# Kernel optimization log

Hardware: AMD Instinct MI355X
Metric: run time of the kernel (lower is better)

## Reference

```python
import jax, jax.numpy as jnp
import numpy as np

EPS = 1e-10


def setup_inputs() -> dict:
    key = jax.random.key(0)
    k1, k2, k3 = jax.random.split(key, 3)
    N, D, K = 16384, 512, 8192
    x = jax.random.normal(k1, (N, D), dtype=jnp.float32)
    # trunc_normal(std=0.2) init approximated by clipped normal
    codebook = jnp.clip(0.2 * jax.random.normal(k2, (K, D), dtype=jnp.float32), -0.4, 0.4)
    gumbel_u = jax.random.uniform(k3, (N, K), dtype=jnp.float32)
    temperature = jnp.float32(0.7)
    return {"x": x, "codebook": codebook, "gumbel_u": gumbel_u, "temperature": temperature}


def reference(x, codebook, gumbel_u, temperature):
    # squared euclidean distance via sum-of-squares + matmul: [N, K]
    x2 = jnp.sum(x * x, axis=1, keepdims=True)              # [N, 1]
    c2 = jnp.sum(codebook * codebook, axis=1)               # [K]
    dist = x2 + c2[None, :] - 2.0 * (x @ codebook.T)        # [N, K]
    ids = jnp.argmax(-dist, axis=1)                         # [N]
    # gumbel-softmax sample over -dist logits
    g = -jnp.log(-jnp.log(gumbel_u + EPS) + EPS)            # gumbel noise [N, K]
    weights = jax.nn.softmax((-dist + g) / temperature, axis=1)
    emb = weights @ codebook                                # [N, D]
    return emb, ids
```

## Files before the change

### kernel.cpp

```cpp
#include <hip/hip_runtime.h>

#define NROWS 16384
#define DIM   512
#define BM    32
#define KTILE 32
#define NT    256
#define KC    8192
#define QCAP  32768
#define MARGIN 0.05f
#define DEFER_THR 8.0f
#define LN2   0.69314718055994531f

typedef _Float16 half8  __attribute__((ext_vector_type(8)));
typedef float    f32x4  __attribute__((ext_vector_type(4)));
typedef unsigned int u32;

#define MFMA(a,b,c) __builtin_amdgcn_mfma_f32_16x16x32_f16(a,b,c,0,0,0)

__device__ __forceinline__ float flog2(float x){ return __builtin_amdgcn_logf(x); }
__device__ __forceinline__ float fexp2(float x){ return __builtin_amdgcn_exp2f(x); }
__device__ __forceinline__ f32x4 ntload4(const float* p){
  return __builtin_nontemporal_load((const f32x4*)p);
}
__device__ __forceinline__ void gload16(const void* g, void* l){
  __builtin_amdgcn_global_load_lds(
      (const __attribute__((address_space(1))) u32*)g,
      (__attribute__((address_space(3))) u32*)l, 16, 0, 0);
}

__device__ __forceinline__ void top2_merge(float& v1, int& i1, float& v2, int& i2,
                                           float bv1, int bi1, float bv2, int bi2) {
  bool takeB = (bv1 > v1) || (bv1 == v1 && bi1 < i1);
  float nv1 = takeB ? bv1 : v1; int ni1 = takeB ? bi1 : i1;
  float cv  = takeB ? v1  : bv1; int ci = takeB ? i1  : bi1;
  float ov2 = takeB ? bv2 : v2;  int oi = takeB ? bi2 : i2;
  bool cb = (cv > ov2) || (cv == ov2 && ci < oi);
  v2 = cb ? cv : ov2; i2 = cb ? ci : oi;
  v1 = nv1; i1 = ni1;
}

__global__ void prep_x(const float* __restrict__ x, _Float16* __restrict__ xh) {
  size_t i = (size_t)(blockIdx.x * blockDim.x + threadIdx.x) * 4;
  f32x4 v = *(const f32x4*)(x + i);
  _Float16 h4[4];
  h4[0] = (_Float16)(2.0f * v[0]); h4[1] = (_Float16)(2.0f * v[1]);
  h4[2] = (_Float16)(2.0f * v[2]); h4[3] = (_Float16)(2.0f * v[3]);
  *(uint2*)(xh + i) = *(uint2*)h4;
}

__global__ void prep_cht(const float* __restrict__ c, _Float16* __restrict__ cht) {
  const int gid = blockIdx.x * 256 + threadIdx.x;
  const int code = gid >> 6, u = gid & 63;
  f32x4 v0 = *(const f32x4*)(c + (size_t)code * DIM + u * 8);
  f32x4 v1 = *(const f32x4*)(c + (size_t)code * DIM + u * 8 + 4);
  half8 h;
#pragma unroll
  for (int q = 0; q < 4; ++q) { h[q] = (_Float16)v0[q]; h[4+q] = (_Float16)v1[q]; }
  const int t = code >> 5, cc = code & 31;
  *(half8*)((char*)cht + (size_t)t * 32768 + cc * 1024 + ((u ^ (cc & 7)) << 4)) = h;
}

__global__ void prep_ctt(const float* __restrict__ c, _Float16* __restrict__ ctt) {
  __shared__ _Float16 lt[64][72];
  const int kb = (blockIdx.x >> 3) * 64;
  const int db = (blockIdx.x & 7) * 64;
  {
    const int r = threadIdx.x >> 2, c4 = threadIdx.x & 3;
#pragma unroll
    for (int j = 0; j < 4; ++j) {
      f32x4 v = *(const f32x4*)(c + (size_t)(kb + r) * DIM + db + c4 * 16 + j * 4);
#pragma unroll
      for (int q = 0; q < 4; ++q) lt[r][c4 * 16 + j * 4 + q] = (_Float16)v[q];
    }
  }
  __syncthreads();
  {
    const int d = threadIdx.x >> 2, ks = threadIdx.x & 3;
    half8 o0, o1;
#pragma unroll
    for (int j = 0; j < 8; ++j) { o0[j] = lt[ks*16 + j][d]; o1[j] = lt[ks*16 + 8 + j][d]; }
    const int dg = db + d;
    const int t = (kb >> 5) + (ks >> 1);
    const int u0 = (ks & 1) * 2;
    char* base = (char*)ctt + (size_t)t * 32768 + (size_t)dg * 64;
    *(half8*)(base + ((u0       ^ (dg & 3)) << 4)) = o0;
    *(half8*)(base + (((u0 + 1) ^ (dg & 3)) << 4)) = o1;
  }
}

__global__ void prep_c2(const float* __restrict__ c, float* __restrict__ c2) {
  const int w = threadIdx.x >> 6, l = threadIdx.x & 63;
  const int code = blockIdx.x * 4 + w;
  double s = 0.0;
  for (int i = l; i < DIM; i += 64) { double v = c[(size_t)code * DIM + i]; s += v * v; }
#pragma unroll
  for (int o = 32; o; o >>= 1) s += __shfl_down(s, o, 64);
  if (l == 0) c2[code] = (float)s;
}

__global__ __launch_bounds__(256, 2) void vq_fused(
    const float* __restrict__ U, const _Float16* __restrict__ Xh,
    const _Float16* __restrict__ CHT, const _Float16* __restrict__ CTT,
    const float* __restrict__ C2, const float* __restrict__ Tp,
    float* __restrict__ emb, float* __restrict__ ids,
    int* __restrict__ fixcnt, int* __restrict__ fixq) {
  __shared__ __align__(16) char smem[71680];
  const int tid = threadIdx.x;
  const int w = tid >> 6, l = tid & 63, l15 = l & 15, l4 = l >> 4;
  const int cs = w & 1, rs = w >> 1;
  const int row0 = blockIdx.x * BM;
  const float c1 = 1.4426950408889634f / Tp[0];
  const char* CHTc = (const char*)CHT;
  const char* CTTc = (const char*)CTT;

  half8 xr[16];
  {
    const _Float16* xb = Xh + (size_t)(row0 + rs*16 + l15) * DIM + l4 * 8;
#pragma unroll
    for (int kc = 0; kc < 16; ++kc) xr[kc] = *(const half8*)(xb + kc * 32);
  }

  const int sxq = l15 & 7;
  const int sxp = (l15 ^ (l15 >> 2)) & 3;
  const int qkb = (cs*16 + l15) * 1024;
  const int prow = rs*16 + l15;

  const float* ub  = U  + (size_t)(row0 + prow) * KC + cs*16 + l4*4;
  const float* c2p = C2 + cs*16 + l4*4;

  f32x4 upre  = ntload4(ub);
  f32x4 c2pre = *(const f32x4*)(c2p);

  {
    const char* g = CHTc + (size_t)(w*64 + l) * 16;
    char* lb = smem + w * 1024;
#pragma unroll
    for (int r = 0; r < 8; ++r) gload16(g + r * 4096, lb + r * 4096);
  }

  f32x4 O[8][2];
#pragma unroll
  for (int a = 0; a < 8; ++a)
#pragma unroll
    for (int b = 0; b < 2; ++b) { O[a][b][0]=0.f; O[a][b][1]=0.f; O[a][b][2]=0.f; O[a][b][3]=0.f; }
  half8 ctf[8];
  float mO[2] = {-3e38f, -3e38f};
  float l_run = 0.f;
  float v1 = -3e38f, v2 = -3e38f; int i1 = 0, i2 = 0;
  float* mtab = (float*)(smem + 69632);

  __syncthreads();

#pragma unroll 1
  for (int t = 0; t < NT; ++t) {
    const char* chc = smem + ((t & 1) << 15);

    if (t < NT - 1) {
      const char* g = CHTc + ((size_t)(t + 1)) * 32768 + (size_t)(w*64 + l) * 16;
      char* lb = smem + (((t + 1) & 1) << 15) + w * 1024;
#pragma unroll
      for (int r = 0; r < 8; ++r) gload16(g + r * 4096, lb + r * 4096);
    }

    f32x4 a0 = {0.f, 0.f, 0.f, 0.f};
#pragma unroll
    for (int kc = 0; kc < 16; ++kc) {
      half8 A0 = *(const half8*)(chc + qkb + (((kc*4 + l4) ^ sxq) << 4));
      a0 = MFMA(A0, xr[kc], a0);
    }

    f32x4 zz; float mw = -3e38f;
    {
      const int cbase = t*32 + cs*16 + l4*4;
#pragma unroll
      for (int r = 0; r < 4; ++r) {
        float s = a0[r] - c2pre[r];
        if (s > v1) { v2 = v1; i2 = i1; v1 = s; i1 = cbase + r; }
        else if (s > v2) { v2 = s; i2 = cbase + r; }
        float li = flog2(upre[r] + 1e-10f);
        float y  = fmaf(li, -LN2, 1e-10f);
        float g  = flog2(y) * (-LN2);
        float z  = (s + g) * c1;
        zz[r] = z;
        mw = fmaxf(mw, z);
      }
    }
    mw = fmaxf(mw, __shfl_xor(mw, 16, 64));
    mw = fmaxf(mw, __shfl_xor(mw, 32, 64));
    if (l < 16) mtab[w*16 + l] = mw;

    asm volatile("s_waitcnt lgkmcnt(0)" ::: "memory");
    __builtin_amdgcn_s_barrier();
    __builtin_amdgcn_sched_barrier(0);

    float alphaO[2];
#pragma unroll
    for (int rt = 0; rt < 2; ++rt) {
      float mt = fmaxf(mtab[(2*rt)*16 + l15], mtab[(2*rt + 1)*16 + l15]);
      float mo = mO[rt];
      float mn = (mt > mo + DEFER_THR) ? mt : mo;
      alphaO[rt] = fexp2(mo - mn);
      mO[rt] = mn;
    }
    const float m_own = rs ? mO[1] : mO[0];
    const float a_own = rs ? alphaO[1] : alphaO[0];

    if (t < NT - 1) {
      upre  = ntload4(ub + (size_t)(t + 1) * 32);
      c2pre = *(const f32x4*)(c2p + (t + 1) * 32);
    }

    {
      char* pcur = smem + 65536 + ((t & 1) << 11);
      float p0 = fexp2(zz[0] - m_own);
      float p1 = fexp2(zz[1] - m_own);
      float p2 = fexp2(zz[2] - m_own);
      float p3 = fexp2(zz[3] - m_own);
      l_run = l_run * a_own + ((p0 + p1) + (p2 + p3));
      const int u = cs*2 + (l4 >> 1);
      union { _Float16 h[4]; uint2 q; } pk;
      pk.h[0] = (_Float16)p0; pk.h[1] = (_Float16)p1;
      pk.h[2] = (_Float16)p2; pk.h[3] = (_Float16)p3;
      *(uint2*)(pcur + prow*64 + ((u ^ sxp) << 4) + ((l4 & 1) << 3)) = pk.q;
    }

    if (t > 0) {
      const char* pprev = smem + 65536 + (((t - 1) & 1) << 11);
      half8 pf0 = *(const half8*)(pprev + l15*64        + ((l4 ^ sxp) << 4));
      half8 pf1 = *(const half8*)(pprev + (16 + l15)*64 + ((l4 ^ sxp) << 4));
#pragma unroll
      for (int dt = 0; dt < 8; ++dt) {
        O[dt][0] = MFMA(ctf[dt], pf0, O[dt][0]);
        O[dt][1] = MFMA(ctf[dt], pf1, O[dt][1]);
      }
    }

#pragma unroll
    for (int dt = 0; dt < 8; ++dt)
      ctf[dt] = *(const half8*)(CTTc + (size_t)t * 32768
                                + (size_t)(w*128 + dt*16 + l15) * 64
                                + ((l4 ^ (l15 & 3)) << 4));

#pragma unroll
    for (int rt = 0; rt < 2; ++rt) {
      if (__any(alphaO[rt] != 1.0f)) {
        const float a_ = alphaO[rt];
#pragma unroll
        for (int dt = 0; dt < 8; ++dt) {
          O[dt][rt][0] *= a_; O[dt][rt][1] *= a_;
          O[dt][rt][2] *= a_; O[dt][rt][3] *= a_;
        }
      }
    }

    __builtin_amdgcn_sched_barrier(0);
    asm volatile("s_waitcnt vmcnt(10) lgkmcnt(0)" ::: "memory");
    __builtin_amdgcn_s_barrier();
    __builtin_amdgcn_sched_barrier(0);
  }

  {
    const char* pprev = smem + 65536 + (((NT - 1) & 1) << 11);
    half8 pf0 = *(const half8*)(pprev + l15*64        + ((l4 ^ sxp) << 4));
    half8 pf1 = *(const half8*)(pprev + (16 + l15)*64 + ((l4 ^ sxp) << 4));
#pragma unroll
    for (int dt = 0; dt < 8; ++dt) {
      O[dt][0] = MFMA(ctf[dt], pf0, O[dt][0]);
      O[dt][1] = MFMA(ctf[dt], pf1, O[dt][1]);
    }
  }

  float lt2 = l_run;
  lt2 += __shfl_xor(lt2, 16, 64);
  lt2 += __shfl_xor(lt2, 32, 64);
  {
    float bv1 = __shfl_xor(v1, 16, 64); int bi1 = __shfl_xor(i1, 16, 64);
    float bv2 = __shfl_xor(v2, 16, 64); int bi2 = __shfl_xor(i2, 16, 64);
    top2_merge(v1, i1, v2, i2, bv1, bi1, bv2, bi2);
    bv1 = __shfl_xor(v1, 32, 64); bi1 = __shfl_xor(i1, 32, 64);
    bv2 = __shfl_xor(v2, 32, 64); bi2 = __shfl_xor(i2, 32, 64);
    top2_merge(v1, i1, v2, i2, bv1, bi1, bv2, bi2);
  }
  float* ltab = (float*)(smem + 69888);
  f32x4* atab = (f32x4*)(smem + 70144);
  if (l < 16) {
    ltab[w*16 + l] = lt2;
    f32x4 pk;
    pk[0] = v1; pk[1] = __int_as_float(i1); pk[2] = v2; pk[3] = __int_as_float(i2);
    atab[w*16 + l] = pk;
  }
  __syncthreads();

  const float invr0 = 1.0f / (ltab[l15] + ltab[16 + l15]);
  const float invr1 = 1.0f / (ltab[32 + l15] + ltab[48 + l15]);

  if (w == 0 && l < 32) {
    const int rt = l >> 4, r15 = l & 15;
    f32x4 A = atab[(2*rt)*16 + r15];
    f32x4 B = atab[(2*rt + 1)*16 + r15];
    float V1 = A[0], V2 = A[2];
    int I1 = __float_as_int(A[1]), I2 = __float_as_int(A[3]);
    top2_merge(V1, I1, V2, I2, B[0], __float_as_int(B[1]), B[2], __float_as_int(B[3]));
    ids[row0 + l] = (float)I1;
    if (V1 - V2 <= MARGIN) {
      int qi = atomicAdd(fixcnt, 1);
      if (qi < QCAP) { fixq[qi*3] = row0 + l; fixq[qi*3 + 1] = I1; fixq[qi*3 + 2] = I2; }
    }
  }

  float* stagef = (float*)smem;
#pragma unroll
  for (int h = 0; h < 2; ++h) {
    __syncthreads();
    const float iv = h ? invr1 : invr0;
#pragma unroll
    for (int dt = 0; dt < 8; ++dt) {
      f32x4 v = O[dt][h];
      v[0] *= iv; v[1] *= iv; v[2] *= iv; v[3] *= iv;
      *(f32x4*)(stagef + l15*520 + w*128 + dt*16 + l4*4) = v;
    }
    __syncthreads();
#pragma unroll
    for (int q = 0; q < 8; ++q) {
      const int c = q*256 + tid;
      const int r_ = c >> 7, col = c & 127;
      f32x4 v = *(const f32x4*)(stagef + r_*520 + col*4);
      __builtin_nontemporal_store(v,
          (f32x4*)(emb + (size_t)(row0 + h*16 + r_)*DIM + col*4));
    }
  }
}

__global__ void vq_fixup(const float* __restrict__ X, const float* __restrict__ C,
                         const int* __restrict__ fixcnt, const int* __restrict__ fixq,
                         float* __restrict__ ids) {
  const int nw = (gridDim.x * blockDim.x) >> 6;
  const int gw = (blockIdx.x * blockDim.x + threadIdx.x) >> 6;
  const int l = threadIdx.x & 63;
  int cnt = *fixcnt; if (cnt > QCAP) cnt = QCAP;
  for (int q = gw; q < cnt; q += nw) {
    const int row = fixq[q*3], a = fixq[q*3 + 1], b = fixq[q*3 + 2];
    double da = 0, ca = 0, db = 0, cb = 0;
    for (int i = l; i < DIM; i += 64) {
      double xv = X[(size_t)row * DIM + i];
      double av = C[(size_t)a * DIM + i];
      double bv = C[(size_t)b * DIM + i];
      da += xv * av; ca += av * av;
      db += xv * bv; cb += bv * bv;
    }
#pragma unroll
    for (int o = 32; o; o >>= 1) {
      da += __shfl_down(da, o, 64); ca += __shfl_down(ca, o, 64);
      db += __shfl_down(db, o, 64); cb += __shfl_down(cb, o, 64);
    }
    if (l == 0) {
      double sa = 2.0 * da - ca, sb = 2.0 * db - cb;
      int win = (sb > sa || (sb == sa && b < a)) ? b : a;
      ids[row] = (float)win;
    }
  }
}

extern "C" void kernel_launch(void* const* d_in, const int* in_sizes, int n_in,
                              void* d_out, int out_size, void* d_ws, size_t ws_size,
                              hipStream_t stream) {
  (void)in_sizes; (void)n_in; (void)out_size; (void)ws_size;
  const float* x  = (const float*)d_in[0];
  const float* cb = (const float*)d_in[1];
  const float* u  = (const float*)d_in[2];
  const float* tp = (const float*)d_in[3];
  float* emb = (float*)d_out;
  float* ids = emb + (size_t)NROWS * DIM;

  char* ws = (char*)d_ws;
  int* fixcnt = (int*)ws;
  int* fixq = (int*)(ws + 256);
  size_t off = (256 + (size_t)QCAP * 12 + 511) & ~(size_t)511;
  _Float16* xh  = (_Float16*)(ws + off); off += (size_t)NROWS * DIM * 2;
  _Float16* cht = (_Float16*)(ws + off); off += (size_t)KC * DIM * 2;
  _Float16* ctt = (_Float16*)(ws + off); off += (size_t)DIM * KC * 2;
  float* c2 = (float*)(ws + off);

  hipMemsetAsync(fixcnt, 0, 4, stream);
  prep_x  <<<(NROWS * DIM) / 1024, 256, 0, stream>>>(x, xh);
  prep_cht<<<(KC * 64) / 256, 256, 0, stream>>>(cb, cht);
  prep_ctt<<<(KC / 64) * (DIM / 64), 256, 0, stream>>>(cb, ctt);
  prep_c2 <<<KC / 4, 256, 0, stream>>>(cb, c2);
  vq_fused<<<NROWS / BM, 256, 0, stream>>>(u, xh, cht, ctt, c2, tp, emb, ids, fixcnt, fixq);
  vq_fixup<<<32, 256, 0, stream>>>(x, cb, fixcnt, fixq, ids);
}
```

Measured before the change: 620.7 us.

## Double row tile to 64 with 512-thread blocks sharing codebook tiles

Doubles the rows per block from 32 to 64 and launches 8 waves per block, so each staged codebook tile in LDS and each CTT fragment is reused across twice as many rows. Each wave now owns 64 output dims across 4 row-tiles, holding an O[4][4] accumulator, and tracks its own softmax max separately. The distance MFMA chain is split into two independent accumulators, and the epilogue writes through per-wave LDS staging with no block-wide sync. In exchange it raises register pressure and shared memory per block, which may reduce occupancy.

```diff
diff --git a/kernel.cpp b/kernel.cpp
--- a/kernel.cpp
+++ b/kernel.cpp
@@ -2,7 +2,7 @@
 
 #define NROWS 16384
 #define DIM   512
-#define BM    32
+#define BM    64
 #define KTILE 32
 #define NT    256
 #define KC    8192
@@ -98,13 +98,13 @@
   if (l == 0) c2[code] = (float)s;
 }
 
-__global__ __launch_bounds__(256, 2) void vq_fused(
+__global__ __launch_bounds__(512, 2) void vq_fused(
     const float* __restrict__ U, const _Float16* __restrict__ Xh,
     const _Float16* __restrict__ CHT, const _Float16* __restrict__ CTT,
     const float* __restrict__ C2, const float* __restrict__ Tp,
     float* __restrict__ emb, float* __restrict__ ids,
     int* __restrict__ fixcnt, int* __restrict__ fixq) {
-  __shared__ __align__(16) char smem[71680];
+  __shared__ __align__(16) char smem[76800];
   const int tid = threadIdx.x;
   const int w = tid >> 6, l = tid & 63, l15 = l & 15, l4 = l >> 4;
   const int cs = w & 1, rs = w >> 1;
@@ -121,9 +121,12 @@
   }
 
   const int sxq = l15 & 7;
+  const int qkb = (cs*16 + l15) * 1024;
+  const int eE = ((l4      ) ^ sxq) << 4;
+  const int eO = ((4 | l4  ) ^ sxq) << 4;
   const int sxp = (l15 ^ (l15 >> 2)) & 3;
-  const int qkb = (cs*16 + l15) * 1024;
   const int prow = rs*16 + l15;
+  const int cxo = (l4 ^ (l15 & 3)) << 4;
 
   const float* ub  = U  + (size_t)(row0 + prow) * KC + cs*16 + l4*4;
   const float* c2p = C2 + cs*16 + l4*4;
@@ -132,22 +135,22 @@
   f32x4 c2pre = *(const f32x4*)(c2p);
 
   {
-    const char* g = CHTc + (size_t)(w*64 + l) * 16;
-    char* lb = smem + w * 1024;
-#pragma unroll
-    for (int r = 0; r < 8; ++r) gload16(g + r * 4096, lb + r * 4096);
-  }
-
-  f32x4 O[8][2];
-#pragma unroll
-  for (int a = 0; a < 8; ++a)
-#pragma unroll
-    for (int b = 0; b < 2; ++b) { O[a][b][0]=0.f; O[a][b][1]=0.f; O[a][b][2]=0.f; O[a][b][3]=0.f; }
-  half8 ctf[8];
-  float mO[2] = {-3e38f, -3e38f};
-  float l_run = 0.f;
+    const char* g = CHTc + (size_t)tid * 16;
+    char* lb = smem + (size_t)tid * 16;
+#pragma unroll
+    for (int r = 0; r < 4; ++r) gload16(g + r * 8192, lb + r * 8192);
+  }
+
+  f32x4 O[4][4];
+#pragma unroll
+  for (int a = 0; a < 4; ++a)
+#pragma unroll
+    for (int b = 0; b < 4; ++b) { O[a][b][0]=0.f; O[a][b][1]=0.f; O[a][b][2]=0.f; O[a][b][3]=0.f; }
+  half8 ctf[4];
+  float mO[4] = {-3e38f, -3e38f, -3e38f, -3e38f};
+  float m_own = -3e38f, l_run = 0.f;
   float v1 = -3e38f, v2 = -3e38f; int i1 = 0, i2 = 0;
-  float* mtab = (float*)(smem + 69632);
+  float* mtab = (float*)(smem + 73728);
 
   __syncthreads();
 
@@ -156,18 +159,28 @@
     const char* chc = smem + ((t & 1) << 15);
 
     if (t < NT - 1) {
-      const char* g = CHTc + ((size_t)(t + 1)) * 32768 + (size_t)(w*64 + l) * 16;
-      char* lb = smem + (((t + 1) & 1) << 15) + w * 1024;
-#pragma unroll
-      for (int r = 0; r < 8; ++r) gload16(g + r * 4096, lb + r * 4096);
-    }
-
-    f32x4 a0 = {0.f, 0.f, 0.f, 0.f};
-#pragma unroll
-    for (int kc = 0; kc < 16; ++kc) {
-      half8 A0 = *(const half8*)(chc + qkb + (((kc*4 + l4) ^ sxq) << 4));
-      a0 = MFMA(A0, xr[kc], a0);
-    }
+      const char* g = CHTc + ((size_t)(t + 1)) * 32768 + (size_t)tid * 16;
+      char* lb = smem + (((t + 1) & 1) << 15) + (size_t)tid * 16;
+#pragma unroll
+      for (int r = 0; r < 4; ++r) gload16(g + r * 8192, lb + r * 8192);
+    }
+    __builtin_amdgcn_sched_barrier(0);
+
+    f32x4 ae = {0.f,0.f,0.f,0.f}, ao = {0.f,0.f,0.f,0.f};
+    {
+      const char* pE = chc + qkb + eE;
+      const char* pO = chc + qkb + eO;
+#pragma unroll
+      for (int j = 0; j < 8; ++j) {
+        half8 AE = *(const half8*)(pE + j * 128);
+        half8 AO = *(const half8*)(pO + j * 128);
+        ae = MFMA(AE, xr[2*j],     ae);
+        ao = MFMA(AO, xr[2*j + 1], ao);
+      }
+    }
+    f32x4 a0;
+    a0[0] = ae[0] + ao[0]; a0[1] = ae[1] + ao[1];
+    a0[2] = ae[2] + ao[2]; a0[3] = ae[3] + ao[3];
 
     f32x4 zz; float mw = -3e38f;
     {
@@ -193,17 +206,21 @@
     __builtin_amdgcn_s_barrier();
     __builtin_amdgcn_sched_barrier(0);
 
-    float alphaO[2];
-#pragma unroll
-    for (int rt = 0; rt < 2; ++rt) {
+    float alphaO[4];
+#pragma unroll
+    for (int rt = 0; rt < 4; ++rt) {
       float mt = fmaxf(mtab[(2*rt)*16 + l15], mtab[(2*rt + 1)*16 + l15]);
       float mo = mO[rt];
       float mn = (mt > mo + DEFER_THR) ? mt : mo;
       alphaO[rt] = fexp2(mo - mn);
       mO[rt] = mn;
     }
-    const float m_own = rs ? mO[1] : mO[0];
-    const float a_own = rs ? alphaO[1] : alphaO[0];
+    {
+      float mt = fmaxf(mtab[(2*rs)*16 + l15], mtab[(2*rs + 1)*16 + l15]);
+      float mn = (mt > m_own + DEFER_THR) ? mt : m_own;
+      l_run *= fexp2(m_own - mn);
+      m_own = mn;
+    }
 
     if (t < NT - 1) {
       upre  = ntload4(ub + (size_t)(t + 1) * 32);
@@ -211,12 +228,12 @@
     }
 
     {
-      char* pcur = smem + 65536 + ((t & 1) << 11);
+      char* pcur = smem + 65536 + ((t & 1) << 12);
       float p0 = fexp2(zz[0] - m_own);
       float p1 = fexp2(zz[1] - m_own);
       float p2 = fexp2(zz[2] - m_own);
       float p3 = fexp2(zz[3] - m_own);
-      l_run = l_run * a_own + ((p0 + p1) + (p2 + p3));
+      l_run += (p0 + p1) + (p2 + p3);
       const int u = cs*2 + (l4 >> 1);
       union { _Float16 h[4]; uint2 q; } pk;
       pk.h[0] = (_Float16)p0; pk.h[1] = (_Float16)p1;
@@ -225,28 +242,31 @@
     }
 
     if (t > 0) {
-      const char* pprev = smem + 65536 + (((t - 1) & 1) << 11);
-      half8 pf0 = *(const half8*)(pprev + l15*64        + ((l4 ^ sxp) << 4));
-      half8 pf1 = *(const half8*)(pprev + (16 + l15)*64 + ((l4 ^ sxp) << 4));
-#pragma unroll
-      for (int dt = 0; dt < 8; ++dt) {
-        O[dt][0] = MFMA(ctf[dt], pf0, O[dt][0]);
-        O[dt][1] = MFMA(ctf[dt], pf1, O[dt][1]);
-      }
-    }
-
-#pragma unroll
-    for (int dt = 0; dt < 8; ++dt)
-      ctf[dt] = *(const half8*)(CTTc + (size_t)t * 32768
-                                + (size_t)(w*128 + dt*16 + l15) * 64
-                                + ((l4 ^ (l15 & 3)) << 4));
-
-#pragma unroll
-    for (int rt = 0; rt < 2; ++rt) {
+      const char* pprev = smem + 65536 + (((t - 1) & 1) << 12);
+      half8 pf[4];
+#pragma unroll
+      for (int rt = 0; rt < 4; ++rt)
+        pf[rt] = *(const half8*)(pprev + (rt*16 + l15)*64 + ((l4 ^ sxp) << 4));
+#pragma unroll
+      for (int dt = 0; dt < 4; ++dt)
+#pragma unroll
+        for (int rt = 0; rt < 4; ++rt)
+          O[dt][rt] = MFMA(ctf[dt], pf[rt], O[dt][rt]);
+    }
+
+    {
+      const char* cb_ = CTTc + (size_t)t * 32768 + (size_t)(w*64 + l15) * 64 + cxo;
+#pragma unroll
+      for (int dt = 0; dt < 4; ++dt)
+        ctf[dt] = *(const half8*)(cb_ + dt * 1024);
+    }
+
+#pragma unroll
+    for (int rt = 0; rt < 4; ++rt) {
       if (__any(alphaO[rt] != 1.0f)) {
         const float a_ = alphaO[rt];
 #pragma unroll
-        for (int dt = 0; dt < 8; ++dt) {
+        for (int dt = 0; dt < 4; ++dt) {
           O[dt][rt][0] *= a_; O[dt][rt][1] *= a_;
           O[dt][rt][2] *= a_; O[dt][rt][3] *= a_;
         }
@@ -254,20 +274,22 @@
     }
 
     __builtin_amdgcn_sched_barrier(0);
-    asm volatile("s_waitcnt vmcnt(10) lgkmcnt(0)" ::: "memory");
+    asm volatile("s_waitcnt vmcnt(6) lgkmcnt(0)" ::: "memory");
     __builtin_amdgcn_s_barrier();
     __builtin_amdgcn_sched_barrier(0);
   }
 
   {
-    const char* pprev = smem + 65536 + (((NT - 1) & 1) << 11);
-    half8 pf0 = *(const half8*)(pprev + l15*64        + ((l4 ^ sxp) << 4));
-    half8 pf1 = *(const half8*)(pprev + (16 + l15)*64 + ((l4 ^ sxp) << 4));
-#pragma unroll
-    for (int dt = 0; dt < 8; ++dt) {
-      O[dt][0] = MFMA(ctf[dt], pf0, O[dt][0]);
-      O[dt][1] = MFMA(ctf[dt], pf1, O[dt][1]);
-    }
+    const char* pprev = smem + 65536 + (((NT - 1) & 1) << 12);
+    half8 pf[4];
+#pragma unroll
+    for (int rt = 0; rt < 4; ++rt)
+      pf[rt] = *(const half8*)(pprev + (rt*16 + l15)*64 + ((l4 ^ sxp) << 4));
+#pragma unroll
+    for (int dt = 0; dt < 4; ++dt)
+#pragma unroll
+      for (int rt = 0; rt < 4; ++rt)
+        O[dt][rt] = MFMA(ctf[dt], pf[rt], O[dt][rt]);
   }
 
   float lt2 = l_run;
@@ -281,8 +303,8 @@
     bv2 = __shfl_xor(v2, 32, 64); bi2 = __shfl_xor(i2, 32, 64);
     top2_merge(v1, i1, v2, i2, bv1, bi1, bv2, bi2);
   }
-  float* ltab = (float*)(smem + 69888);
-  f32x4* atab = (f32x4*)(smem + 70144);
+  float* ltab = (float*)(smem + 74240);
+  f32x4* atab = (f32x4*)(smem + 74752);
   if (l < 16) {
     ltab[w*16 + l] = lt2;
     f32x4 pk;
@@ -291,13 +313,14 @@
   }
   __syncthreads();
 
-  const float invr0 = 1.0f / (ltab[l15] + ltab[16 + l15]);
-  const float invr1 = 1.0f / (ltab[32 + l15] + ltab[48 + l15]);
-
-  if (w == 0 && l < 32) {
-    const int rt = l >> 4, r15 = l & 15;
-    f32x4 A = atab[(2*rt)*16 + r15];
-    f32x4 B = atab[(2*rt + 1)*16 + r15];
+  float inv4[4];
+#pragma unroll
+  for (int rt = 0; rt < 4; ++rt)
+    inv4[rt] = 1.0f / (ltab[(2*rt)*16 + l15] + ltab[(2*rt + 1)*16 + l15]);
+
+  if (w == 0) {
+    f32x4 A = atab[(2*(l >> 4))*16 + (l & 15)];
+    f32x4 B = atab[(2*(l >> 4) + 1)*16 + (l & 15)];
     float V1 = A[0], V2 = A[2];
     int I1 = __float_as_int(A[1]), I2 = __float_as_int(A[3]);
     top2_merge(V1, I1, V2, I2, B[0], __float_as_int(B[1]), B[2], __float_as_int(B[3]));
@@ -308,25 +331,28 @@
     }
   }
 
-  float* stagef = (float*)smem;
+  char* wbase = smem + w * 9216;
 #pragma unroll
   for (int h = 0; h < 2; ++h) {
-    __syncthreads();
-    const float iv = h ? invr1 : invr0;
-#pragma unroll
-    for (int dt = 0; dt < 8; ++dt) {
-      f32x4 v = O[dt][h];
-      v[0] *= iv; v[1] *= iv; v[2] *= iv; v[3] *= iv;
-      *(f32x4*)(stagef + l15*520 + w*128 + dt*16 + l4*4) = v;
-    }
-    __syncthreads();
-#pragma unroll
-    for (int q = 0; q < 8; ++q) {
-      const int c = q*256 + tid;
-      const int r_ = c >> 7, col = c & 127;
-      f32x4 v = *(const f32x4*)(stagef + r_*520 + col*4);
-      __builtin_nontemporal_store(v,
-          (f32x4*)(emb + (size_t)(row0 + h*16 + r_)*DIM + col*4));
+#pragma unroll
+    for (int rtl = 0; rtl < 2; ++rtl) {
+      const int rt = 2*h + rtl;
+      const int lrow = rtl*16 + l15;
+#pragma unroll
+      for (int dt = 0; dt < 4; ++dt)
+#pragma unroll
+        for (int r = 0; r < 4; ++r) {
+          const int dloc = dt*16 + l4*4 + r;
+          *(float*)(wbase + (lrow*72 + dloc)*4) = O[dt][rt][r] * inv4[rt];
+        }
+    }
+    __builtin_amdgcn_s_waitcnt(0);
+#pragma unroll
+    for (int ir = 0; ir < 8; ++ir) {
+      const int lrow = ir*4 + l4;
+      f32x4 vv = *(const f32x4*)(wbase + (lrow*72 + l15*4)*4);
+      __builtin_nontemporal_store(vv,
+          (f32x4*)(emb + (size_t)(row0 + h*32 + lrow)*DIM + w*64 + l15*4));
     }
   }
 }
@@ -386,6 +412,6 @@
   prep_cht<<<(KC * 64) / 256, 256, 0, stream>>>(cb, cht);
   prep_ctt<<<(KC / 64) * (DIM / 64), 256, 0, stream>>>(cb, ctt);
   prep_c2 <<<KC / 4, 256, 0, stream>>>(cb, c2);
-  vq_fused<<<NROWS / BM, 256, 0, stream>>>(u, xh, cht, ctt, c2, tp, emb, ids, fixcnt, fixq);
+  vq_fused<<<NROWS / BM, 512, 0, stream>>>(u, xh, cht, ctt, c2, tp, emb, ids, fixcnt, fixq);
   vq_fixup<<<32, 256, 0, stream>>>(x, cb, fixcnt, fixq, ids);
 }
```

Result: no change. 631.0 us (+1.7%).

## Load codebook fragments directly into registers instead of staging through LDS

Applied to the files above, without the earlier changes.

The fp16 codebook tile is re-laid out in the prep kernel so that each lane can load its MFMA A-fragments straight from global memory into registers. These registers are prefetched one tile ahead, replacing the double-buffered global_load_lds path and cutting shared memory from about 70KB to about 39KB. The distance MFMA chain is split into two independent accumulators to shorten the dependency chain. The cost is 16 extra half8 registers per lane and global latency exposed through register prefetch, with possible register pressure under the 2-waves launch bound. Two waves per column slice now fetch the same data from global or L2 rather than sharing one LDS copy.

```diff
diff --git a/kernel.cpp b/kernel.cpp
--- a/kernel.cpp
+++ b/kernel.cpp
@@ -3,7 +3,6 @@
 #define NROWS 16384
 #define DIM   512
 #define BM    32
-#define KTILE 32
 #define NT    256
 #define KC    8192
 #define QCAP  32768
@@ -13,7 +12,6 @@
 
 typedef _Float16 half8  __attribute__((ext_vector_type(8)));
 typedef float    f32x4  __attribute__((ext_vector_type(4)));
-typedef unsigned int u32;
 
 #define MFMA(a,b,c) __builtin_amdgcn_mfma_f32_16x16x32_f16(a,b,c,0,0,0)
 
@@ -21,11 +19,6 @@
 __device__ __forceinline__ float fexp2(float x){ return __builtin_amdgcn_exp2f(x); }
 __device__ __forceinline__ f32x4 ntload4(const float* p){
   return __builtin_nontemporal_load((const f32x4*)p);
-}
-__device__ __forceinline__ void gload16(const void* g, void* l){
-  __builtin_amdgcn_global_load_lds(
-      (const __attribute__((address_space(1))) u32*)g,
-      (__attribute__((address_space(3))) u32*)l, 16, 0, 0);
 }
 
 __device__ __forceinline__ void top2_merge(float& v1, int& i1, float& v2, int& i2,
@@ -48,7 +41,7 @@
   *(uint2*)(xh + i) = *(uint2*)h4;
 }
 
-__global__ void prep_cht(const float* __restrict__ c, _Float16* __restrict__ cht) {
+__global__ void prep_cht2(const float* __restrict__ c, _Float16* __restrict__ cht) {
   const int gid = blockIdx.x * 256 + threadIdx.x;
   const int code = gid >> 6, u = gid & 63;
   f32x4 v0 = *(const f32x4*)(c + (size_t)code * DIM + u * 8);
@@ -56,8 +49,8 @@
   half8 h;
 #pragma unroll
   for (int q = 0; q < 4; ++q) { h[q] = (_Float16)v0[q]; h[4+q] = (_Float16)v1[q]; }
-  const int t = code >> 5, cc = code & 31;
-  *(half8*)((char*)cht + (size_t)t * 32768 + cc * 1024 + ((u ^ (cc & 7)) << 4)) = h;
+  const int t = code >> 5, cc = code & 31, kc = u >> 2, ul = u & 3;
+  *(half8*)((char*)cht + (size_t)t * 32768 + kc * 2048 + cc * 64 + ul * 16) = h;
 }
 
 __global__ void prep_ctt(const float* __restrict__ c, _Float16* __restrict__ ctt) {
@@ -100,17 +93,17 @@
 
 __global__ __launch_bounds__(256, 2) void vq_fused(
     const float* __restrict__ U, const _Float16* __restrict__ Xh,
-    const _Float16* __restrict__ CHT, const _Float16* __restrict__ CTT,
+    const _Float16* __restrict__ CHT2, const _Float16* __restrict__ CTT,
     const float* __restrict__ C2, const float* __restrict__ Tp,
     float* __restrict__ emb, float* __restrict__ ids,
     int* __restrict__ fixcnt, int* __restrict__ fixq) {
-  __shared__ __align__(16) char smem[71680];
+  __shared__ __align__(16) char smem[39936];
   const int tid = threadIdx.x;
   const int w = tid >> 6, l = tid & 63, l15 = l & 15, l4 = l >> 4;
   const int cs = w & 1, rs = w >> 1;
   const int row0 = blockIdx.x * BM;
   const float c1 = 1.4426950408889634f / Tp[0];
-  const char* CHTc = (const char*)CHT;
+  const char* CH2c = (const char*)CHT2;
   const char* CTTc = (const char*)CTT;
 
   half8 xr[16];
@@ -120,10 +113,9 @@
     for (int kc = 0; kc < 16; ++kc) xr[kc] = *(const half8*)(xb + kc * 32);
   }
 
-  const int sxq = l15 & 7;
   const int sxp = (l15 ^ (l15 >> 2)) & 3;
-  const int qkb = (cs*16 + l15) * 1024;
   const int prow = rs*16 + l15;
+  const int afo = (cs*16 + l15) * 64 + l4*16;
 
   const float* ub  = U  + (size_t)(row0 + prow) * KC + cs*16 + l4*4;
   const float* c2p = C2 + cs*16 + l4*4;
@@ -131,12 +123,10 @@
   f32x4 upre  = ntload4(ub);
   f32x4 c2pre = *(const f32x4*)(c2p);
 
-  {
-    const char* g = CHTc + (size_t)(w*64 + l) * 16;
-    char* lb = smem + w * 1024;
-#pragma unroll
-    for (int r = 0; r < 8; ++r) gload16(g + r * 4096, lb + r * 4096);
-  }
+  half8 af[16];
+#pragma unroll
+  for (int kc = 0; kc < 16; ++kc)
+    af[kc] = *(const half8*)(CH2c + kc * 2048 + afo);
 
   f32x4 O[8][2];
 #pragma unroll
@@ -147,26 +137,28 @@
   float mO[2] = {-3e38f, -3e38f};
   float l_run = 0.f;
   float v1 = -3e38f, v2 = -3e38f; int i1 = 0, i2 = 0;
-  float* mtab = (float*)(smem + 69632);
+  float* mtab = (float*)(smem + 37888);
 
   __syncthreads();
 
 #pragma unroll 1
   for (int t = 0; t < NT; ++t) {
-    const char* chc = smem + ((t & 1) << 15);
-
-    if (t < NT - 1) {
-      const char* g = CHTc + ((size_t)(t + 1)) * 32768 + (size_t)(w*64 + l) * 16;
-      char* lb = smem + (((t + 1) & 1) << 15) + w * 1024;
-#pragma unroll
-      for (int r = 0; r < 8; ++r) gload16(g + r * 4096, lb + r * 4096);
-    }
-
-    f32x4 a0 = {0.f, 0.f, 0.f, 0.f};
-#pragma unroll
-    for (int kc = 0; kc < 16; ++kc) {
-      half8 A0 = *(const half8*)(chc + qkb + (((kc*4 + l4) ^ sxq) << 4));
-      a0 = MFMA(A0, xr[kc], a0);
+    f32x4 ae = {0.f,0.f,0.f,0.f}, ao = {0.f,0.f,0.f,0.f};
+#pragma unroll
+    for (int j = 0; j < 8; ++j) {
+      ae = MFMA(af[2*j],     xr[2*j],     ae);
+      ao = MFMA(af[2*j + 1], xr[2*j + 1], ao);
+    }
+    f32x4 a0;
+    a0[0] = ae[0] + ao[0]; a0[1] = ae[1] + ao[1];
+    a0[2] = ae[2] + ao[2]; a0[3] = ae[3] + ao[3];
+
+    {
+      const int tn = (t < NT - 1) ? t + 1 : t;
+      const char* gb = CH2c + (size_t)tn * 32768 + afo;
+#pragma unroll
+      for (int kc = 0; kc < 16; ++kc)
+        af[kc] = *(const half8*)(gb + kc * 2048);
     }
 
     f32x4 zz; float mw = -3e38f;
@@ -211,7 +203,7 @@
     }
 
     {
-      char* pcur = smem + 65536 + ((t & 1) << 11);
+      char* pcur = smem + ((t & 1) << 11);
       float p0 = fexp2(zz[0] - m_own);
       float p1 = fexp2(zz[1] - m_own);
       float p2 = fexp2(zz[2] - m_own);
@@ -225,7 +217,7 @@
     }
 
     if (t > 0) {
-      const char* pprev = smem + 65536 + (((t - 1) & 1) << 11);
+      const char* pprev = smem + (((t - 1) & 1) << 11);
       half8 pf0 = *(const half8*)(pprev + l15*64        + ((l4 ^ sxp) << 4));
       half8 pf1 = *(const half8*)(pprev + (16 + l15)*64 + ((l4 ^ sxp) << 4));
 #pragma unroll
@@ -254,13 +246,13 @@
     }
 
     __builtin_amdgcn_sched_barrier(0);
-    asm volatile("s_waitcnt vmcnt(10) lgkmcnt(0)" ::: "memory");
+    asm volatile("s_waitcnt lgkmcnt(0)" ::: "memory");
     __builtin_amdgcn_s_barrier();
     __builtin_amdgcn_sched_barrier(0);
   }
 
   {
-    const char* pprev = smem + 65536 + (((NT - 1) & 1) << 11);
+    const char* pprev = smem + (((NT - 1) & 1) << 11);
     half8 pf0 = *(const half8*)(pprev + l15*64        + ((l4 ^ sxp) << 4));
     half8 pf1 = *(const half8*)(pprev + (16 + l15)*64 + ((l4 ^ sxp) << 4));
 #pragma unroll
@@ -281,8 +273,8 @@
     bv2 = __shfl_xor(v2, 32, 64); bi2 = __shfl_xor(i2, 32, 64);
     top2_merge(v1, i1, v2, i2, bv1, bi1, bv2, bi2);
   }
-  float* ltab = (float*)(smem + 69888);
-  f32x4* atab = (f32x4*)(smem + 70144);
+  float* ltab = (float*)(smem + 38144);
+  f32x4* atab = (f32x4*)(smem + 38400);
   if (l < 16) {
     ltab[w*16 + l] = lt2;
     f32x4 pk;
@@ -308,7 +300,7 @@
     }
   }
 
-  float* stagef = (float*)smem;
+  float* stagef = (float*)(smem + 4096);
 #pragma unroll
   for (int h = 0; h < 2; ++h) {
     __syncthreads();
@@ -376,16 +368,16 @@
   int* fixcnt = (int*)ws;
   int* fixq = (int*)(ws + 256);
   size_t off = (256 + (size_t)QCAP * 12 + 511) & ~(size_t)511;
-  _Float16* xh  = (_Float16*)(ws + off); off += (size_t)NROWS * DIM * 2;
-  _Float16* cht = (_Float16*)(ws + off); off += (size_t)KC * DIM * 2;
-  _Float16* ctt = (_Float16*)(ws + off); off += (size_t)DIM * KC * 2;
+  _Float16* xh   = (_Float16*)(ws + off); off += (size_t)NROWS * DIM * 2;
+  _Float16* cht2 = (_Float16*)(ws + off); off += (size_t)KC * DIM * 2;
+  _Float16* ctt  = (_Float16*)(ws + off); off += (size_t)DIM * KC * 2;
   float* c2 = (float*)(ws + off);
 
   hipMemsetAsync(fixcnt, 0, 4, stream);
-  prep_x  <<<(NROWS * DIM) / 1024, 256, 0, stream>>>(x, xh);
-  prep_cht<<<(KC * 64) / 256, 256, 0, stream>>>(cb, cht);
-  prep_ctt<<<(KC / 64) * (DIM / 64), 256, 0, stream>>>(cb, ctt);
-  prep_c2 <<<KC / 4, 256, 0, stream>>>(cb, c2);
-  vq_fused<<<NROWS / BM, 256, 0, stream>>>(u, xh, cht, ctt, c2, tp, emb, ids, fixcnt, fixq);
+  prep_x   <<<(NROWS * DIM) / 1024, 256, 0, stream>>>(x, xh);
+  prep_cht2<<<(KC * 64) / 256, 256, 0, stream>>>(cb, cht2);
+  prep_ctt <<<(KC / 64) * (DIM / 64), 256, 0, stream>>>(cb, ctt);
+  prep_c2  <<<KC / 4, 256, 0, stream>>>(cb, c2);
+  vq_fused<<<NROWS / BM, 256, 0, stream>>>(u, xh, cht2, ctt, c2, tp, emb, ids, fixcnt, fixq);
   vq_fixup<<<32, 256, 0, stream>>>(x, cb, fixcnt, fixq, ids);
 }
```

After: 1.058 ms. 1.7x slower.

## Software-pipeline softmax by one tile to drop a barrier; fold temperature into inputs

Applied to the files above, without the earlier changes.

The main loop is restructured so each tile's exp/P write and running-max rescale happen one iteration later, using a double-buffered max table. That lets the kernel keep a single barrier per iteration instead of two. The 1/T·log2e scale is also folded into the fp16 x copy and into c2, which removes a multiply per logit. The costs are more live registers (z_prev), a longer epilogue, and fp16 rounding of x·scale, which changes precision slightly. The fixup margin is rescaled to match the new units.

```diff
diff --git a/kernel.cpp b/kernel.cpp
--- a/kernel.cpp
+++ b/kernel.cpp
@@ -3,7 +3,6 @@
 #define NROWS 16384
 #define DIM   512
 #define BM    32
-#define KTILE 32
 #define NT    256
 #define KC    8192
 #define QCAP  32768
@@ -39,12 +38,14 @@
   v1 = nv1; i1 = ni1;
 }
 
-__global__ void prep_x(const float* __restrict__ x, _Float16* __restrict__ xh) {
+__global__ void prep_x(const float* __restrict__ x, const float* __restrict__ Tp,
+                       _Float16* __restrict__ xh) {
+  const float s2 = 2.0f * 1.4426950408889634f / Tp[0];
   size_t i = (size_t)(blockIdx.x * blockDim.x + threadIdx.x) * 4;
   f32x4 v = *(const f32x4*)(x + i);
   _Float16 h4[4];
-  h4[0] = (_Float16)(2.0f * v[0]); h4[1] = (_Float16)(2.0f * v[1]);
-  h4[2] = (_Float16)(2.0f * v[2]); h4[3] = (_Float16)(2.0f * v[3]);
+  h4[0] = (_Float16)(s2 * v[0]); h4[1] = (_Float16)(s2 * v[1]);
+  h4[2] = (_Float16)(s2 * v[2]); h4[3] = (_Float16)(s2 * v[3]);
   *(uint2*)(xh + i) = *(uint2*)h4;
 }
 
@@ -88,14 +89,15 @@
   }
 }
 
-__global__ void prep_c2(const float* __restrict__ c, float* __restrict__ c2) {
+__global__ void prep_c2(const float* __restrict__ c, const float* __restrict__ Tp,
+                        float* __restrict__ c2) {
   const int w = threadIdx.x >> 6, l = threadIdx.x & 63;
   const int code = blockIdx.x * 4 + w;
   double s = 0.0;
   for (int i = l; i < DIM; i += 64) { double v = c[(size_t)code * DIM + i]; s += v * v; }
 #pragma unroll
   for (int o = 32; o; o >>= 1) s += __shfl_down(s, o, 64);
-  if (l == 0) c2[code] = (float)s;
+  if (l == 0) c2[code] = (float)s * (1.4426950408889634f / Tp[0]);
 }
 
 __global__ __launch_bounds__(256, 2) void vq_fused(
@@ -110,6 +112,7 @@
   const int cs = w & 1, rs = w >> 1;
   const int row0 = blockIdx.x * BM;
   const float c1 = 1.4426950408889634f / Tp[0];
+  const float tinv = 1.0f / Tp[0];
   const char* CHTc = (const char*)CHT;
   const char* CTTc = (const char*)CTT;
 
@@ -144,24 +147,63 @@
 #pragma unroll
     for (int b = 0; b < 2; ++b) { O[a][b][0]=0.f; O[a][b][1]=0.f; O[a][b][2]=0.f; O[a][b][3]=0.f; }
   half8 ctf[8];
+  f32x4 z_prev;
   float mO[2] = {-3e38f, -3e38f};
   float l_run = 0.f;
   float v1 = -3e38f, v2 = -3e38f; int i1 = 0, i2 = 0;
-  float* mtab = (float*)(smem + 69632);
 
   __syncthreads();
 
 #pragma unroll 1
   for (int t = 0; t < NT; ++t) {
+    float alphaO[2] = {1.0f, 1.0f};
+    if (t > 0) {
+      const float* mt_ = (const float*)(smem + 69632 + (((t - 1) & 1) << 8));
+#pragma unroll
+      for (int rt = 0; rt < 2; ++rt) {
+        float m2 = fmaxf(mt_[(2*rt)*16 + l15], mt_[(2*rt + 1)*16 + l15]);
+        float mo = mO[rt];
+        float mn = (m2 > mo + DEFER_THR) ? m2 : mo;
+        alphaO[rt] = fexp2(mo - mn);
+        mO[rt] = mn;
+      }
+      l_run *= (rs ? alphaO[1] : alphaO[0]);
+    }
+    const float m_own = rs ? mO[1] : mO[0];
+
+    if (t >= 2) {
+      const char* pprev = smem + 65536 + ((t & 1) << 11);
+      half8 pf0 = *(const half8*)(pprev + l15*64        + ((l4 ^ sxp) << 4));
+      half8 pf1 = *(const half8*)(pprev + (16 + l15)*64 + ((l4 ^ sxp) << 4));
+#pragma unroll
+      for (int dt = 0; dt < 8; ++dt) {
+        O[dt][0] = MFMA(ctf[dt], pf0, O[dt][0]);
+        O[dt][1] = MFMA(ctf[dt], pf1, O[dt][1]);
+      }
+    }
+
+    {
+      const int tc = (t > 0) ? t - 1 : 0;
+#pragma unroll
+      for (int dt = 0; dt < 8; ++dt)
+        ctf[dt] = *(const half8*)(CTTc + (size_t)tc * 32768
+                                  + (size_t)(w*128 + dt*16 + l15) * 64
+                                  + ((l4 ^ (l15 & 3)) << 4));
+    }
+
+#pragma unroll
+    for (int rt = 0; rt < 2; ++rt) {
+      if (__any(alphaO[rt] != 1.0f)) {
+        const float a_ = alphaO[rt];
+#pragma unroll
+        for (int dt = 0; dt < 8; ++dt) {
+          O[dt][rt][0] *= a_; O[dt][rt][1] *= a_;
+          O[dt][rt][2] *= a_; O[dt][rt][3] *= a_;
+        }
+      }
+    }
+
     const char* chc = smem + ((t & 1) << 15);
-
-    if (t < NT - 1) {
-      const char* g = CHTc + ((size_t)(t + 1)) * 32768 + (size_t)(w*64 + l) * 16;
-      char* lb = smem + (((t + 1) & 1) << 15) + w * 1024;
-#pragma unroll
-      for (int r = 0; r < 8; ++r) gload16(g + r * 4096, lb + r * 4096);
-    }
-
     f32x4 a0 = {0.f, 0.f, 0.f, 0.f};
 #pragma unroll
     for (int kc = 0; kc < 16; ++kc) {
@@ -179,53 +221,65 @@
         else if (s > v2) { v2 = s; i2 = cbase + r; }
         float li = flog2(upre[r] + 1e-10f);
         float y  = fmaf(li, -LN2, 1e-10f);
-        float g  = flog2(y) * (-LN2);
-        float z  = (s + g) * c1;
+        float z  = fmaf(flog2(y), -tinv, s);
         zz[r] = z;
         mw = fmaxf(mw, z);
       }
     }
     mw = fmaxf(mw, __shfl_xor(mw, 16, 64));
     mw = fmaxf(mw, __shfl_xor(mw, 32, 64));
-    if (l < 16) mtab[w*16 + l] = mw;
-
-    asm volatile("s_waitcnt lgkmcnt(0)" ::: "memory");
-    __builtin_amdgcn_s_barrier();
-    __builtin_amdgcn_sched_barrier(0);
-
-    float alphaO[2];
-#pragma unroll
-    for (int rt = 0; rt < 2; ++rt) {
-      float mt = fmaxf(mtab[(2*rt)*16 + l15], mtab[(2*rt + 1)*16 + l15]);
-      float mo = mO[rt];
-      float mn = (mt > mo + DEFER_THR) ? mt : mo;
-      alphaO[rt] = fexp2(mo - mn);
-      mO[rt] = mn;
-    }
-    const float m_own = rs ? mO[1] : mO[0];
-    const float a_own = rs ? alphaO[1] : alphaO[0];
-
-    if (t < NT - 1) {
-      upre  = ntload4(ub + (size_t)(t + 1) * 32);
-      c2pre = *(const f32x4*)(c2p + (t + 1) * 32);
-    }
-
-    {
-      char* pcur = smem + 65536 + ((t & 1) << 11);
-      float p0 = fexp2(zz[0] - m_own);
-      float p1 = fexp2(zz[1] - m_own);
-      float p2 = fexp2(zz[2] - m_own);
-      float p3 = fexp2(zz[3] - m_own);
-      l_run = l_run * a_own + ((p0 + p1) + (p2 + p3));
+
+    if (l < 16) ((float*)(smem + 69632 + ((t & 1) << 8)))[w*16 + l] = mw;
+
+    if (t > 0) {
+      char* pcur = smem + 65536 + (((t - 1) & 1) << 11);
+      float p0 = fexp2(z_prev[0] - m_own);
+      float p1 = fexp2(z_prev[1] - m_own);
+      float p2 = fexp2(z_prev[2] - m_own);
+      float p3 = fexp2(z_prev[3] - m_own);
+      l_run += (p0 + p1) + (p2 + p3);
       const int u = cs*2 + (l4 >> 1);
       union { _Float16 h[4]; uint2 q; } pk;
       pk.h[0] = (_Float16)p0; pk.h[1] = (_Float16)p1;
       pk.h[2] = (_Float16)p2; pk.h[3] = (_Float16)p3;
       *(uint2*)(pcur + prow*64 + ((u ^ sxp) << 4) + ((l4 & 1) << 3)) = pk.q;
     }
-
-    if (t > 0) {
-      const char* pprev = smem + 65536 + (((t - 1) & 1) << 11);
+    z_prev = zz;
+
+    if (t < NT - 1) {
+      const char* g = CHTc + ((size_t)(t + 1)) * 32768 + (size_t)(w*64 + l) * 16;
+      char* lb = smem + (((t + 1) & 1) << 15) + w * 1024;
+#pragma unroll
+      for (int r = 0; r < 8; ++r) gload16(g + r * 4096, lb + r * 4096);
+    }
+
+    if (t < NT - 1) {
+      upre  = ntload4(ub + (size_t)(t + 1) * 32);
+      c2pre = *(const f32x4*)(c2p + (t + 1) * 32);
+    }
+
+    __builtin_amdgcn_sched_barrier(0);
+    asm volatile("s_waitcnt vmcnt(2) lgkmcnt(0)" ::: "memory");
+    __builtin_amdgcn_s_barrier();
+    __builtin_amdgcn_sched_barrier(0);
+  }
+
+  {
+    float alphaO[2];
+    const float* mt_ = (const float*)(smem + 69632 + (((NT - 1) & 1) << 8));
+#pragma unroll
+    for (int rt = 0; rt < 2; ++rt) {
+      float m2 = fmaxf(mt_[(2*rt)*16 + l15], mt_[(2*rt + 1)*16 + l15]);
+      float mo = mO[rt];
+      float mn = (m2 > mo + DEFER_THR) ? m2 : mo;
+      alphaO[rt] = fexp2(mo - mn);
+      mO[rt] = mn;
+    }
+    l_run *= (rs ? alphaO[1] : alphaO[0]);
+    const float m_own = rs ? mO[1] : mO[0];
+
+    {
+      const char* pprev = smem + 65536 + ((NT & 1) << 11);
       half8 pf0 = *(const half8*)(pprev + l15*64        + ((l4 ^ sxp) << 4));
       half8 pf1 = *(const half8*)(pprev + (16 + l15)*64 + ((l4 ^ sxp) << 4));
 #pragma unroll
@@ -234,13 +288,11 @@
         O[dt][1] = MFMA(ctf[dt], pf1, O[dt][1]);
       }
     }
-
 #pragma unroll
     for (int dt = 0; dt < 8; ++dt)
-      ctf[dt] = *(const half8*)(CTTc + (size_t)t * 32768
+      ctf[dt] = *(const half8*)(CTTc + (size_t)(NT - 1) * 32768
                                 + (size_t)(w*128 + dt*16 + l15) * 64
                                 + ((l4 ^ (l15 & 3)) << 4));
-
 #pragma unroll
     for (int rt = 0; rt < 2; ++rt) {
       if (__any(alphaO[rt] != 1.0f)) {
@@ -252,21 +304,30 @@
         }
       }
     }
-
-    __builtin_amdgcn_sched_barrier(0);
-    asm volatile("s_waitcnt vmcnt(10) lgkmcnt(0)" ::: "memory");
+    {
+      char* pcur = smem + 65536 + (((NT - 1) & 1) << 11);
+      float p0 = fexp2(z_prev[0] - m_own);
+      float p1 = fexp2(z_prev[1] - m_own);
+      float p2 = fexp2(z_prev[2] - m_own);
+      float p3 = fexp2(z_prev[3] - m_own);
+      l_run += (p0 + p1) + (p2 + p3);
+      const int u = cs*2 + (l4 >> 1);
+      union { _Float16 h[4]; uint2 q; } pk;
+      pk.h[0] = (_Float16)p0; pk.h[1] = (_Float16)p1;
+      pk.h[2] = (_Float16)p2; pk.h[3] = (_Float16)p3;
+      *(uint2*)(pcur + prow*64 + ((u ^ sxp) << 4) + ((l4 & 1) << 3)) = pk.q;
+    }
+    asm volatile("s_waitcnt lgkmcnt(0)" ::: "memory");
     __builtin_amdgcn_s_barrier();
-    __builtin_amdgcn_sched_barrier(0);
-  }
-
-  {
-    const char* pprev = smem + 65536 + (((NT - 1) & 1) << 11);
-    half8 pf0 = *(const half8*)(pprev + l15*64        + ((l4 ^ sxp) << 4));
-    half8 pf1 = *(const half8*)(pprev + (16 + l15)*64 + ((l4 ^ sxp) << 4));
-#pragma unroll
-    for (int dt = 0; dt < 8; ++dt) {
-      O[dt][0] = MFMA(ctf[dt], pf0, O[dt][0]);
-      O[dt][1] = MFMA(ctf[dt], pf1, O[dt][1]);
+    {
+      const char* pprev = smem + 65536 + (((NT - 1) & 1) << 11);
+      half8 pf0 = *(const half8*)(pprev + l15*64        + ((l4 ^ sxp) << 4));
+      half8 pf1 = *(const half8*)(pprev + (16 + l15)*64 + ((l4 ^ sxp) << 4));
+#pragma unroll
+      for (int dt = 0; dt < 8; ++dt) {
+        O[dt][0] = MFMA(ctf[dt], pf0, O[dt][0]);
+        O[dt][1] = MFMA(ctf[dt], pf1, O[dt][1]);
+      }
     }
   }
 
@@ -281,8 +342,9 @@
     bv2 = __shfl_xor(v2, 32, 64); bi2 = __shfl_xor(i2, 32, 64);
     top2_merge(v1, i1, v2, i2, bv1, bi1, bv2, bi2);
   }
-  float* ltab = (float*)(smem + 69888);
-  f32x4* atab = (f32x4*)(smem + 70144);
+  float* ltab = (float*)(smem + 70144);
+  f32x4* atab = (f32x4*)(smem + 70400);
+  __syncthreads();
   if (l < 16) {
     ltab[w*16 + l] = lt2;
     f32x4 pk;
@@ -302,7 +364,7 @@
     int I1 = __float_as_int(A[1]), I2 = __float_as_int(A[3]);
     top2_merge(V1, I1, V2, I2, B[0], __float_as_int(B[1]), B[2], __float_as_int(B[3]));
     ids[row0 + l] = (float)I1;
-    if (V1 - V2 <= MARGIN) {
+    if (V1 - V2 <= MARGIN * c1) {
       int qi = atomicAdd(fixcnt, 1);
       if (qi < QCAP) { fixq[qi*3] = row0 + l; fixq[qi*3 + 1] = I1; fixq[qi*3 + 2] = I2; }
     }
@@ -382,10 +444,10 @@
   float* c2 = (float*)(ws + off);
 
   hipMemsetAsync(fixcnt, 0, 4, stream);
-  prep_x  <<<(NROWS * DIM) / 1024, 256, 0, stream>>>(x, xh);
+  prep_x  <<<(NROWS * DIM) / 1024, 256, 0, stream>>>(x, tp, xh);
   prep_cht<<<(KC * 64) / 256, 256, 0, stream>>>(cb, cht);
   prep_ctt<<<(KC / 64) * (DIM / 64), 256, 0, stream>>>(cb, ctt);
-  prep_c2 <<<KC / 4, 256, 0, stream>>>(cb, c2);
+  prep_c2 <<<KC / 4, 256, 0, stream>>>(cb, tp, c2);
   vq_fused<<<NROWS / BM, 256, 0, stream>>>(u, xh, cht, ctt, c2, tp, emb, ids, fixcnt, fixq);
   vq_fixup<<<32, 256, 0, stream>>>(x, cb, fixcnt, fixq, ids);
 }
```

Result: faster. 608.0 us (-2.1%).
